# Performance work log

Hardware: AMD Instinct MI355X
Metric: run time of the kernel (lower is better)

## Reference

```python
import jax, jax.numpy as jnp
import numpy as np

CHEB_K = 3  # matches init_kwargs


def setup_inputs() -> dict:
    key = jax.random.key(0)
    k1, k2, k3, k4 = jax.random.split(key, 4)
    B, N, C_IN, C_OUT, D = 64, 4000, 64, 64, 10
    x = jax.random.normal(k1, (B, N, C_IN), dtype=jnp.float32)
    node_emb = jax.random.normal(k2, (N, D), dtype=jnp.float32)
    weights_pool = jax.random.normal(k3, (D, CHEB_K, C_IN, C_OUT), dtype=jnp.float32) * 0.1
    bias_pool = jax.random.normal(k4, (D, C_OUT), dtype=jnp.float32) * 0.1
    return {"x": x, "node_emb": node_emb, "weights_pool": weights_pool, "bias_pool": bias_pool}


def reference(x, node_emb, weights_pool, bias_pool):
    # adpadj == 'agcrn': adaptive adjacency from node embeddings
    N = node_emb.shape[0]
    supports = jax.nn.softmax(jax.nn.relu(node_emb @ node_emb.T), axis=1)  # [N,N]
    # Chebyshev polynomial basis: T0=I, T1=A, Tk = 2A Tk-1 - Tk-2
    support_set = [jnp.eye(N, dtype=x.dtype), supports]
    for _ in range(2, CHEB_K):
        support_set.append(2.0 * supports @ support_set[-1] - support_set[-2])
    S = jnp.stack(support_set, axis=0)  # [K,N,N]
    # per-node generated weights and bias
    weights = jnp.einsum('nd,dkio->nkio', node_emb, weights_pool)  # [N,K,Cin,Cout]
    bias = node_emb @ bias_pool  # [N,Cout]
    # graph conv: aggregate neighbors for each Chebyshev order, then per-node matmul
    x_g = jnp.einsum('knm,bmc->bnkc', S, x)  # [B,N,K,Cin]
    out = jnp.einsum('bnki,nkio->bno', x_g, weights) + bias  # [B,N,Cout]
    return out
```

## Files before the change

### kernel.cpp

```cpp
#include <hip/hip_runtime.h>

typedef __attribute__((ext_vector_type(8))) __bf16 bf16x8;
typedef __attribute__((ext_vector_type(4))) float f32x4;
typedef __attribute__((ext_vector_type(8))) unsigned short u16x8;
typedef __attribute__((ext_vector_type(4))) unsigned short u16x4;

#define N_NODES 4000
#define LD 4096
#define D_EMB 10
#define NT 64

__device__ __forceinline__ unsigned short f2bf(float f) {
  union { float f; unsigned int u; } v; v.f = f;
  unsigned int r = v.u + 0x7fffu + ((v.u >> 16) & 1u);
  return (unsigned short)(r >> 16);
}
__device__ __forceinline__ float bf2f(unsigned short s) {
  union { unsigned int u; float f; } v; v.u = ((unsigned int)s) << 16;
  return v.f;
}

#define AS1 __attribute__((address_space(1)))
#define AS3 __attribute__((address_space(3)))
__device__ __forceinline__ void gll16(const void* g, void* l) {
  __builtin_amdgcn_global_load_lds((const AS1 void*)g, (AS3 void*)l, 16, 0, 0);
}

__global__ __launch_bounds__(256) void transpose_x_kernel(const float* __restrict__ x,
                                                          unsigned short* __restrict__ Xc) {
  __shared__ float tl[64 * 65];
  const int t = threadIdx.x;
  const int m0 = blockIdx.x * 64;
  const int b = blockIdx.y;
#pragma unroll
  for (int rep = 0; rep < 16; ++rep) {
    int idx = rep * 256 + t;
    int ml = idx >> 6, c = idx & 63;
    int m = m0 + ml;
    tl[ml * 65 + c] = (m < N_NODES) ? x[(b * N_NODES + m) * 64 + c] : 0.f;
  }
  __syncthreads();
  const int c_out = t >> 2, q = t & 3;
  u16x8 v0, v1;
#pragma unroll
  for (int j = 0; j < 8; ++j) v0[j] = f2bf(tl[(q * 16 + j) * 65 + c_out]);
#pragma unroll
  for (int j = 0; j < 8; ++j) v1[j] = f2bf(tl[(q * 16 + 8 + j) * 65 + c_out]);
  unsigned short* dst = Xc + (size_t)(b * 64 + c_out) * LD + m0 + q * 16;
  *(u16x8*)dst = v0;
  *(u16x8*)(dst + 8) = v1;
}

__global__ __launch_bounds__(256) void build_adj_kernel(const float* __restrict__ emb,
                                                        unsigned short* __restrict__ A) {
  __shared__ float e_lds[N_NODES];
  __shared__ float embn[16];
  __shared__ float red[16];
  const int n = blockIdx.x, t = threadIdx.x;
  if (n >= N_NODES) {
    for (int m = t; m < LD; m += 256) A[(size_t)n * LD + m] = 0;
    return;
  }
  if (t < D_EMB) embn[t] = emb[n * D_EMB + t];
  __syncthreads();
  float lsum = 0.f;
  for (int m = t; m < N_NODES; m += 256) {
    float dot = 0.f;
#pragma unroll
    for (int d = 0; d < D_EMB; ++d) dot += embn[d] * emb[m * D_EMB + d];
    float e = __expf(fmaxf(dot, 0.f));
    e_lds[m] = e;
    lsum += e;
  }
#pragma unroll
  for (int off = 32; off > 0; off >>= 1) lsum += __shfl_down(lsum, off, 64);
  const int lane = t & 63, wave = t >> 6;
  if (lane == 0) red[wave] = lsum;
  __syncthreads();
  if (t == 0) red[8] = 1.f / (red[0] + red[1] + red[2] + red[3]);
  __syncthreads();
  const float inv = red[8];
  for (int m = t; m < LD; m += 256) {
    float v = (m < N_NODES) ? e_lds[m] * inv : 0.f;
    A[(size_t)n * LD + m] = f2bf(v);
  }
}

__global__ __launch_bounds__(256) void wpt_kernel(const float* __restrict__ wp,
                                                  unsigned short* __restrict__ wpT) {
  __shared__ float tl[64 * 65];
  const int dk = blockIdx.x;
  const int d = dk / 3, k = dk % 3;
  const float* src = wp + (size_t)dk * 4096;
  const int t = threadIdx.x;
#pragma unroll
  for (int rep = 0; rep < 16; ++rep) {
    int idx = rep * 256 + t;
    tl[(idx >> 6) * 65 + (idx & 63)] = src[idx];
  }
  __syncthreads();
#pragma unroll
  for (int rep = 0; rep < 16; ++rep) {
    int idx = rep * 256 + t;
    int o = idx >> 6, i = idx & 63;
    wpT[(size_t)d * 12288 + o * 192 + k * 64 + i] = f2bf(tl[i * 65 + o]);
  }
}

__global__ __launch_bounds__(256) void wgen_kernel(const float* __restrict__ emb,
                                                   const unsigned short* __restrict__ wpT,
                                                   unsigned short* __restrict__ W_all) {
  __shared__ float el[50 * D_EMB];
  const int t = threadIdx.x;
  const int j = blockIdx.x * 256 + t;
  const int n0 = blockIdx.y * 50;
  for (int idx = t; idx < 50 * D_EMB; idx += 256) el[idx] = emb[n0 * D_EMB + idx];
  __syncthreads();
  float w[D_EMB];
#pragma unroll
  for (int d = 0; d < D_EMB; ++d) w[d] = bf2f(wpT[(size_t)d * 12288 + j]);
  for (int n = 0; n < 50; ++n) {
    float a = 0.f;
#pragma unroll
    for (int d = 0; d < D_EMB; ++d) a += el[n * D_EMB + d] * w[d];
    W_all[(size_t)(n0 + n) * 12288 + j] = f2bf(a);
  }
}

template <bool WRITE_T>
__global__ __launch_bounds__(512, 2) void gemm256_kernel(const unsigned short* __restrict__ Amat,
                                                         const unsigned short* __restrict__ Bmat,
                                                         unsigned short* __restrict__ Cn,
                                                         unsigned short* __restrict__ Ct) {
  __shared__ __align__(128) char smem[131072];
  const int tid = threadIdx.x;
  const int wave = tid >> 6, lane = tid & 63;
  const int wr = wave >> 2, wc = wave & 3;
  const int bm = blockIdx.y * 256, bn = blockIdx.x * 256;
  const int l15 = lane & 15, quad = lane >> 4;
  const int swz = (lane & 7) << 4;
  const int k0 = (quad * 16) ^ swz;
  const int k1 = (64 + quad * 16) ^ swz;

  const char* Ard = smem + (wr * 128 + l15) * 128;
  const char* Brd = smem + 65536 + (wc * 64 + l15) * 128;

  const int u = tid >> 3;
  const int xc = ((tid & 7) ^ (u & 7)) << 3;
  const unsigned short* gA = Amat + (size_t)(bm + u) * LD + xc;
  const unsigned short* gB = Bmat + (size_t)(bn + (u >> 5) * 64 + (u & 31)) * LD + xc;
  char* dA = smem + wave * 1024;
  char* dB = smem + 65536 + (wave >> 2) * 8192 + (wave & 3) * 1024;

#define STAGE_A(P, H, KT) do { \
    gll16(gA + (size_t)((H) * 64) * LD + (KT) * 64,       dA + (P) * 32768 + (H) * 8192); \
    gll16(gA + (size_t)((H) * 64 + 128) * LD + (KT) * 64, dA + (P) * 32768 + (H) * 8192 + 16384); \
  } while (0)
#define STAGE_B(P, H, KT) do { \
    gll16(gB + (size_t)((H) * 32) * LD + (KT) * 64,       dB + (P) * 32768 + (H) * 4096); \
    gll16(gB + (size_t)((H) * 32 + 128) * LD + (KT) * 64, dB + (P) * 32768 + (H) * 4096 + 16384); \
  } while (0)
#define BAR __builtin_amdgcn_s_barrier()
#define LGKM0 asm volatile("s_waitcnt lgkmcnt(0)" ::: "memory")
#define VM10 asm volatile("s_waitcnt vmcnt(10)" ::: "memory")

  f32x4 acc[8][4] = {};
  bf16x8 a[4][2], b0[2][2], b1[2][2];

#define READ_A(MH, P) do { \
    _Pragma("unroll") for (int m = 0; m < 4; ++m) { \
      a[m][0] = *(const bf16x8*)(Ard + (P) * 32768 + ((MH) * 4 + m) * 2048 + k0); \
      a[m][1] = *(const bf16x8*)(Ard + (P) * 32768 + ((MH) * 4 + m) * 2048 + k1); } } while (0)
#define READ_B(BR, NH, P) do { \
    _Pragma("unroll") for (int n = 0; n < 2; ++n) { \
      BR[n][0] = *(const bf16x8*)(Brd + (P) * 32768 + ((NH) * 2 + n) * 2048 + k0); \
      BR[n][1] = *(const bf16x8*)(Brd + (P) * 32768 + ((NH) * 2 + n) * 2048 + k1); } } while (0)
#define MFMA16(MH, BR, NH) do { \
    _Pragma("unroll") for (int m = 0; m < 4; ++m) \
      _Pragma("unroll") for (int n = 0; n < 2; ++n) { \
        f32x4 c = acc[(MH) * 4 + m][(NH) * 2 + n]; \
        c = __builtin_amdgcn_mfma_f32_16x16x32_bf16(a[m][0], BR[n][0], c, 0, 0, 0); \
        c = __builtin_amdgcn_mfma_f32_16x16x32_bf16(a[m][1], BR[n][1], c, 0, 0, 0); \
        acc[(MH) * 4 + m][(NH) * 2 + n] = c; } } while (0)

  STAGE_A(0, 0, 0);
  STAGE_B(0, 0, 0);
  STAGE_B(0, 1, 0);
  STAGE_A(0, 1, 0);
  STAGE_A(1, 0, 1);
  STAGE_B(1, 0, 1);
  STAGE_B(1, 1, 1);
  VM10;
  BAR;

#define TILE(T, P, Q) do { \
    const int kt1 = ((T) + 1 < NT) ? (T) + 1 : 0;  \
    const int kt2 = ((T) + 2 < NT) ? (T) + 2 : 0; \
     \
    READ_A(0, P); READ_B(b0, 0, P); \
    STAGE_A(Q, 1, kt1); \
    BAR; LGKM0; \
    __builtin_amdgcn_s_setprio(1); MFMA16(0, b0, 0); __builtin_amdgcn_s_setprio(0); \
    VM10; BAR; \
     \
    READ_B(b1, 1, P); \
    STAGE_A(P, 0, kt2); \
    BAR; LGKM0; \
    __builtin_amdgcn_s_setprio(1); MFMA16(0, b1, 1); __builtin_amdgcn_s_setprio(0); \
    VM10; BAR; \
     \
    READ_A(1, P); \
    STAGE_B(P, 0, kt2); \
    BAR; LGKM0; \
    __builtin_amdgcn_s_setprio(1); MFMA16(1, b0, 0); __builtin_amdgcn_s_setprio(0); \
    BAR; \
     \
    STAGE_B(P, 1, kt2); \
    BAR; LGKM0; \
    __builtin_amdgcn_s_setprio(1); MFMA16(1, b1, 1); __builtin_amdgcn_s_setprio(0); \
    VM10; BAR; \
  } while (0)

  for (int t = 0; t < NT; t += 2) {
    TILE(t, 0, 1);
    TILE(t + 1, 1, 0);
  }

#pragma unroll
  for (int mt = 0; mt < 8; ++mt)
#pragma unroll
    for (int nt = 0; nt < 4; ++nt) {
      const int row0 = bm + wr * 128 + mt * 16 + quad * 4;
      const int col = bn + wc * 64 + nt * 16 + l15;
#pragma unroll
      for (int r = 0; r < 4; ++r)
        Cn[(size_t)(row0 + r) * LD + col] = f2bf(acc[mt][nt][r]);
    }

  if (WRITE_T) {
    unsigned short* tr = (unsigned short*)smem;
    asm volatile("s_waitcnt vmcnt(0)" ::: "memory");
    __syncthreads();
#pragma unroll
    for (int ch = 0; ch < 2; ++ch) {
      if ((wc >> 1) == ch) {
#pragma unroll
        for (int mt = 0; mt < 8; ++mt)
#pragma unroll
          for (int nt = 0; nt < 4; ++nt) {
            const int coll = (wc & 1) * 64 + nt * 16 + l15;
            const int row0 = wr * 128 + mt * 16 + quad * 4;
#pragma unroll
            for (int r = 0; r < 4; ++r)
              tr[coll * 264 + row0 + r] = f2bf(acc[mt][nt][r]);
          }
      }
      __syncthreads();
      {
        const int coll = tid >> 2, seg = tid & 3;
        const unsigned short* src = tr + coll * 264 + seg * 64;
        unsigned short* dst = Ct + (size_t)(bn + ch * 128 + coll) * LD + bm + seg * 64;
#pragma unroll
        for (int j = 0; j < 8; ++j)
          *(u16x8*)(dst + j * 8) = *(const u16x8*)(src + j * 8);
      }
      __syncthreads();
    }
  } else {
    asm volatile("s_waitcnt vmcnt(0)" ::: "memory");
  }
#undef TILE
#undef MFMA16
#undef READ_B
#undef READ_A
#undef VM10
#undef LGKM0
#undef BAR
#undef STAGE_B
#undef STAGE_A
}

#define EST 200
__global__ __launch_bounds__(256) void epilogue_kernel(const float* __restrict__ x,
                                                       const float* __restrict__ emb,
                                                       const unsigned short* __restrict__ W_all,
                                                       const float* __restrict__ bp,
                                                       const unsigned short* __restrict__ Y1,
                                                       const unsigned short* __restrict__ Y2,
                                                       float* __restrict__ out) {
  __shared__ unsigned short Wt[64 * EST];
  __shared__ unsigned short xg[64 * EST];
  __shared__ float embn[16];
  const int n = blockIdx.x, t = threadIdx.x;
  if (t < D_EMB) embn[t] = emb[n * D_EMB + t];

  {
    const int o = t >> 2, sub = t & 3;
    const unsigned short* srcW = W_all + (size_t)n * 12288 + o * 192 + sub * 48;
    unsigned short* dstW = Wt + o * EST + sub * 48;
#pragma unroll
    for (int c = 0; c < 6; ++c)
      *(u16x8*)(dstW + c * 8) = *(const u16x8*)(srcW + c * 8);
  }
  for (int idx = t; idx < 1024; idx += 256) {
    int b = idx >> 4, c4 = (idx & 15) * 4;
    f32x4 v = *(const f32x4*)(x + (size_t)(b * N_NODES + n) * 64 + c4);
    u16x4 s;
#pragma unroll
    for (int j = 0; j < 4; ++j) s[j] = f2bf(v[j]);
    *(u16x4*)(xg + b * EST + c4) = s;
  }
  for (int idx = t; idx < 512; idx += 256) {
    int b = idx >> 3, c8 = (idx & 7) * 8;
    *(u16x8*)(xg + b * EST + 64 + c8) = *(const u16x8*)(Y1 + (size_t)n * LD + b * 64 + c8);
  }
  __syncthreads();
  for (int idx = t; idx < 512; idx += 256) {
    int b = idx >> 3, c8 = (idx & 7) * 8;
    u16x8 y2 = *(const u16x8*)(Y2 + (size_t)n * LD + b * 64 + c8);
    u16x8 r;
#pragma unroll
    for (int j = 0; j < 8; ++j)
      r[j] = f2bf(2.f * bf2f(y2[j]) - bf2f(xg[b * EST + c8 + j]));
    *(u16x8*)(xg + b * EST + 128 + c8) = r;
  }
  __syncthreads();

  const int wave = t >> 6, lane = t & 63, quad = lane >> 4;
  const unsigned short* Apx = xg + (wave * 16 + (lane & 15)) * EST + quad * 8;
  f32x4 acc[4] = {};
#pragma unroll
  for (int step = 0; step < 6; ++step) {
    int koff = step * 32;
    bf16x8 a = *(const bf16x8*)(Apx + koff);
#pragma unroll
    for (int nt = 0; nt < 4; ++nt) {
      bf16x8 bfr = *(const bf16x8*)(Wt + (nt * 16 + (lane & 15)) * EST + quad * 8 + koff);
      acc[nt] = __builtin_amdgcn_mfma_f32_16x16x32_bf16(a, bfr, acc[nt], 0, 0, 0);
    }
  }
  float bias[4];
#pragma unroll
  for (int nt = 0; nt < 4; ++nt) {
    float a = 0.f;
#pragma unroll
    for (int d = 0; d < D_EMB; ++d) a += embn[d] * bp[d * 64 + nt * 16 + (lane & 15)];
    bias[nt] = a;
  }
#pragma unroll
  for (int nt = 0; nt < 4; ++nt)
#pragma unroll
    for (int rr = 0; rr < 4; ++rr) {
      int b_row = wave * 16 + quad * 4 + rr;
      out[(size_t)(b_row * N_NODES + n) * 64 + nt * 16 + (lane & 15)] = acc[nt][rr] + bias[nt];
    }
}

extern "C" void kernel_launch(void* const* d_in, const int* in_sizes, int n_in,
                              void* d_out, int out_size, void* d_ws, size_t ws_size,
                              hipStream_t stream) {
  const float* x   = (const float*)d_in[0];
  const float* emb = (const float*)d_in[1];
  const float* wp  = (const float*)d_in[2];
  const float* bp  = (const float*)d_in[3];
  float* out = (float*)d_out;

  const size_t S = (size_t)LD * LD;
  unsigned short* Y1    = (unsigned short*)d_ws;
  unsigned short* Y2    = Y1 + S;
  unsigned short* Xc    = Y1 + 2 * S;
  unsigned short* Am    = Y1 + 3 * S;
  unsigned short* Y1t   = Y1 + 4 * S;
  unsigned short* wpT   = Xc;
  unsigned short* W_all = Xc + 256 * 1024;

  transpose_x_kernel<<<dim3(64, 64), 256, 0, stream>>>(x, Xc);
  build_adj_kernel<<<LD, 256, 0, stream>>>(emb, Am);
  gemm256_kernel<true ><<<dim3(16, 16), 512, 0, stream>>>(Am, Xc, Y1, Y1t);
  gemm256_kernel<false><<<dim3(16, 16), 512, 0, stream>>>(Am, Y1t, Y2, nullptr);
  wpt_kernel<<<30, 256, 0, stream>>>(wp, wpT);
  wgen_kernel<<<dim3(48, 80), 256, 0, stream>>>(emb, wpT, W_all);
  epilogue_kernel<<<N_NODES, 256, 0, stream>>>(x, emb, W_all, bp, Y1, Y2, out);
}
```

Baseline: 475.7 us.

## Restructure GEMM LDS layout into k-split halves with 4x4 MFMA phases

Reorganizes the 256x256 bf16 GEMM's shared-memory staging so each k-tile is split into two 32-wide k halves with 64-byte rows and a new XOR swizzle. Each phase now issues a 4x4 block of single MFMAs per k-half, where before it issued 4x2 blocks of paired MFMAs. This changes the load and prefetch schedule and the vmcnt waits. The aim is fewer LDS reads per MFMA and better overlap of global-to-LDS loads with compute. It risks bank conflicts from the new swizzle and subtle hazards in the reordered stage and wait counts.

Result: slower. 486.4 us (+2.2%).

```diff
diff --git a/kernel.cpp b/kernel.cpp
--- a/kernel.cpp
+++ b/kernel.cpp
@@ -138,92 +138,83 @@
   const int wr = wave >> 2, wc = wave & 3;
   const int bm = blockIdx.y * 256, bn = blockIdx.x * 256;
   const int l15 = lane & 15, quad = lane >> 4;
-  const int swz = (lane & 7) << 4;
-  const int k0 = (quad * 16) ^ swz;
-  const int k1 = (64 + quad * 16) ^ swz;
-
-  const char* Ard = smem + (wr * 128 + l15) * 128;
-  const char* Brd = smem + 65536 + (wc * 64 + l15) * 128;
-
-  const int u = tid >> 3;
-  const int xc = ((tid & 7) ^ (u & 7)) << 3;
-  const unsigned short* gA = Amat + (size_t)(bm + u) * LD + xc;
-  const unsigned short* gB = Bmat + (size_t)(bn + (u >> 5) * 64 + (u & 31)) * LD + xc;
+  const int slotb = ((quad ^ ((l15 >> 1) & 3)) << 4);
+
+  const char* Ard = smem + (wr * 128 + l15) * 64 + slotb;
+  const char* Brd = smem + 65536 + (wc * 64 + l15) * 64 + slotb;
+
+  const int u2 = tid >> 2;
+  const int kseg = (tid & 3) ^ ((u2 >> 1) & 3);
+  const unsigned short* gA = Amat + (size_t)(bm + u2) * LD + kseg * 8;
+  const unsigned short* gB = Bmat + (size_t)(bn + u2) * LD + kseg * 8;
   char* dA = smem + wave * 1024;
-  char* dB = smem + 65536 + (wave >> 2) * 8192 + (wave & 3) * 1024;
-
-#define STAGE_A(P, H, KT) do { \
-    gll16(gA + (size_t)((H) * 64) * LD + (KT) * 64,       dA + (P) * 32768 + (H) * 8192); \
-    gll16(gA + (size_t)((H) * 64 + 128) * LD + (KT) * 64, dA + (P) * 32768 + (H) * 8192 + 16384); \
+  char* dB = smem + 65536 + wave * 1024;
+
+#define STAGE_A(P, KS, KT) do { \
+    gll16(gA + (KT) * 64 + (KS) * 32,                      dA + (P) * 32768 + (KS) * 16384); \
+    gll16(gA + (size_t)128 * LD + (KT) * 64 + (KS) * 32,   dA + (P) * 32768 + (KS) * 16384 + 8192); \
   } while (0)
-#define STAGE_B(P, H, KT) do { \
-    gll16(gB + (size_t)((H) * 32) * LD + (KT) * 64,       dB + (P) * 32768 + (H) * 4096); \
-    gll16(gB + (size_t)((H) * 32 + 128) * LD + (KT) * 64, dB + (P) * 32768 + (H) * 4096 + 16384); \
+#define STAGE_B(P, KS, KT) do { \
+    gll16(gB + (KT) * 64 + (KS) * 32,                      dB + (P) * 32768 + (KS) * 16384); \
+    gll16(gB + (size_t)128 * LD + (KT) * 64 + (KS) * 32,   dB + (P) * 32768 + (KS) * 16384 + 8192); \
   } while (0)
 #define BAR __builtin_amdgcn_s_barrier()
 #define LGKM0 asm volatile("s_waitcnt lgkmcnt(0)" ::: "memory")
+#define VM4  asm volatile("s_waitcnt vmcnt(4)" ::: "memory")
+#define VM8  asm volatile("s_waitcnt vmcnt(8)" ::: "memory")
 #define VM10 asm volatile("s_waitcnt vmcnt(10)" ::: "memory")
 
   f32x4 acc[8][4] = {};
-  bf16x8 a[4][2], b0[2][2], b1[2][2];
-
-#define READ_A(MH, P) do { \
-    _Pragma("unroll") for (int m = 0; m < 4; ++m) { \
-      a[m][0] = *(const bf16x8*)(Ard + (P) * 32768 + ((MH) * 4 + m) * 2048 + k0); \
-      a[m][1] = *(const bf16x8*)(Ard + (P) * 32768 + ((MH) * 4 + m) * 2048 + k1); } } while (0)
-#define READ_B(BR, NH, P) do { \
-    _Pragma("unroll") for (int n = 0; n < 2; ++n) { \
-      BR[n][0] = *(const bf16x8*)(Brd + (P) * 32768 + ((NH) * 2 + n) * 2048 + k0); \
-      BR[n][1] = *(const bf16x8*)(Brd + (P) * 32768 + ((NH) * 2 + n) * 2048 + k1); } } while (0)
-#define MFMA16(MH, BR, NH) do { \
-    _Pragma("unroll") for (int m = 0; m < 4; ++m) \
-      _Pragma("unroll") for (int n = 0; n < 2; ++n) { \
-        f32x4 c = acc[(MH) * 4 + m][(NH) * 2 + n]; \
-        c = __builtin_amdgcn_mfma_f32_16x16x32_bf16(a[m][0], BR[n][0], c, 0, 0, 0); \
-        c = __builtin_amdgcn_mfma_f32_16x16x32_bf16(a[m][1], BR[n][1], c, 0, 0, 0); \
-        acc[(MH) * 4 + m][(NH) * 2 + n] = c; } } while (0)
-
+  bf16x8 af[4], bf[4];
+
+#define READ_AF(P, KS, MH) do { _Pragma("unroll") for (int m = 0; m < 4; ++m) \
+    af[m] = *(const bf16x8*)(Ard + (P) * 32768 + (KS) * 16384 + (MH) * 4096 + m * 1024); } while (0)
+#define READ_BF(P, KS) do { _Pragma("unroll") for (int n = 0; n < 4; ++n) \
+    bf[n] = *(const bf16x8*)(Brd + (P) * 32768 + (KS) * 16384 + n * 1024); } while (0)
+#define MFMA4x4(MH) do { _Pragma("unroll") for (int m = 0; m < 4; ++m) \
+    _Pragma("unroll") for (int n = 0; n < 4; ++n) \
+      acc[(MH) * 4 + m][n] = __builtin_amdgcn_mfma_f32_16x16x32_bf16(af[m], bf[n], acc[(MH) * 4 + m][n], 0, 0, 0); } while (0)
+
+  STAGE_B(0, 0, 0);
   STAGE_A(0, 0, 0);
-  STAGE_B(0, 0, 0);
+  STAGE_A(0, 1, 0);
+  STAGE_B(1, 0, 1);
+  STAGE_A(1, 0, 1);
   STAGE_B(0, 1, 0);
-  STAGE_A(0, 1, 0);
-  STAGE_A(1, 0, 1);
-  STAGE_B(1, 0, 1);
-  STAGE_B(1, 1, 1);
-  VM10;
+  VM8;
   BAR;
 
-#define TILE(T, P, Q) do { \
-    const int kt1 = ((T) + 1 < NT) ? (T) + 1 : 0;  \
-    const int kt2 = ((T) + 2 < NT) ? (T) + 2 : 0; \
+#define TILE(T, P) do { \
      \
-    READ_A(0, P); READ_B(b0, 0, P); \
-    STAGE_A(Q, 1, kt1); \
+    READ_AF(P, 0, 0); READ_BF(P, 0); \
+    STAGE_A((P) ^ 1, 1, ((T) + 1 < NT ? (T) + 1 : 0)); \
     BAR; LGKM0; \
-    __builtin_amdgcn_s_setprio(1); MFMA16(0, b0, 0); __builtin_amdgcn_s_setprio(0); \
-    VM10; BAR; \
-     \
-    READ_B(b1, 1, P); \
-    STAGE_A(P, 0, kt2); \
-    BAR; LGKM0; \
-    __builtin_amdgcn_s_setprio(1); MFMA16(0, b1, 1); __builtin_amdgcn_s_setprio(0); \
-    VM10; BAR; \
-     \
-    READ_A(1, P); \
-    STAGE_B(P, 0, kt2); \
-    BAR; LGKM0; \
-    __builtin_amdgcn_s_setprio(1); MFMA16(1, b0, 0); __builtin_amdgcn_s_setprio(0); \
+    __builtin_amdgcn_s_setprio(1); MFMA4x4(0); __builtin_amdgcn_s_setprio(0); \
     BAR; \
      \
-    STAGE_B(P, 1, kt2); \
+    READ_AF(P, 0, 1); \
+    STAGE_B(P, 0, ((T) + 2 < NT ? (T) + 2 : 0)); \
     BAR; LGKM0; \
-    __builtin_amdgcn_s_setprio(1); MFMA16(1, b1, 1); __builtin_amdgcn_s_setprio(0); \
+    __builtin_amdgcn_s_setprio(1); MFMA4x4(1); __builtin_amdgcn_s_setprio(0); \
+    VM4; BAR; \
+     \
+    READ_AF(P, 1, 0); READ_BF(P, 1); \
+    STAGE_A(P, 0, ((T) + 2 < NT ? (T) + 2 : 0)); \
+    BAR; LGKM0; \
+    __builtin_amdgcn_s_setprio(1); MFMA4x4(0); __builtin_amdgcn_s_setprio(0); \
+    BAR; \
+     \
+    READ_AF(P, 1, 1); \
+    STAGE_B((P) ^ 1, 1, ((T) + 1 < NT ? (T) + 1 : 0)); \
+    BAR; LGKM0; \
+    __builtin_amdgcn_s_setprio(1); MFMA4x4(1); __builtin_amdgcn_s_setprio(0); \
     VM10; BAR; \
   } while (0)
 
+#pragma unroll 1
   for (int t = 0; t < NT; t += 2) {
-    TILE(t, 0, 1);
-    TILE(t + 1, 1, 0);
+    TILE(t, 0);
+    TILE(t + 1, 1);
   }
 
 #pragma unroll
@@ -270,10 +261,12 @@
     asm volatile("s_waitcnt vmcnt(0)" ::: "memory");
   }
 #undef TILE
-#undef MFMA16
-#undef READ_B
-#undef READ_A
+#undef MFMA4x4
+#undef READ_BF
+#undef READ_AF
 #undef VM10
+#undef VM8
+#undef VM4
 #undef LGKM0
 #undef BAR
 #undef STAGE_B
```
